# Optimization experiments

Measured on AMD Instinct MI355X. Metric: run time of the kernel, lower is better.

Reference implementation:

```python
import jax, jax.numpy as jnp
import numpy as np

HIDDEN = 1024
HEADS = 16
HEAD_DIM = HIDDEN // HEADS
EPS = 1e-5


def setup_inputs() -> dict:
    key = jax.random.key(0)
    ks = jax.random.split(key, 8)
    B, S, D = 2, 2048, HIDDEN
    s = 1.0 / np.sqrt(D)
    return {
        "x": jax.random.normal(ks[0], (B, S, D), dtype=jnp.float32),
        "Wq": jax.random.uniform(ks[1], (D, D), jnp.float32, -s, s),
        "bq": jnp.zeros((D,), jnp.float32),
        "Wk": jax.random.uniform(ks[2], (D, D), jnp.float32, -s, s),
        "bk": jnp.zeros((D,), jnp.float32),
        "Wv": jax.random.uniform(ks[3], (D, D), jnp.float32, -s, s),
        "bv": jnp.zeros((D,), jnp.float32),
        "gamma": jnp.ones((D,), jnp.float32),
        "beta": jnp.zeros((D,), jnp.float32),
    }


def reference(x, Wq, bq, Wk, bk, Wv, bv, gamma, beta):
    B, S, D = x.shape
    H, Hd = HEADS, HEAD_DIM
    # QKV projections -> [B, H, S, Hd]
    q = (x @ Wq + bq).reshape(B, S, H, Hd).transpose(0, 2, 1, 3)
    k = (x @ Wk + bk).reshape(B, S, H, Hd).transpose(0, 2, 1, 3)
    v = (x @ Wv + bv).reshape(B, S, H, Hd).transpose(0, 2, 1, 3)
    scores = jnp.einsum('bhqd,bhkd->bhqk', q, k) / np.sqrt(Hd).astype(np.float32)
    attn = jax.nn.softmax(scores, axis=-1)  # dropout identity in eval
    ctx = jnp.einsum('bhqk,bhkd->bhqd', attn, v)
    ctx = ctx.transpose(0, 2, 1, 3).reshape(B, S, D)
    y = x + ctx
    mu = jnp.mean(y, axis=-1, keepdims=True)
    var = jnp.var(y, axis=-1, keepdims=True)
    out = (y - mu) * jax.lax.rsqrt(var + EPS) * gamma + beta
    return out, attn.mean(axis=1)
```

## Files before the change

kernel.cpp:

```cpp
#include <hip/hip_runtime.h>

#define S_LEN 2048
#define DIM   1024
#define NH    16
#define HD    64

typedef __bf16 bf16x8 __attribute__((ext_vector_type(8)));
typedef __bf16 bf16x4 __attribute__((ext_vector_type(4)));
typedef float  f32x4  __attribute__((ext_vector_type(4)));
typedef float  f32x16 __attribute__((ext_vector_type(16)));
typedef unsigned int u32x4 __attribute__((ext_vector_type(4)));

#define SCALE_Q (0.125f * 1.44269504088896f)

#define GLOAD_LDS16(g, l) __builtin_amdgcn_global_load_lds( \
    (const __attribute__((address_space(1))) void*)(g),     \
    (__attribute__((address_space(3))) void*)(l), 16, 0, 0)

static __device__ __forceinline__ unsigned cvt_pk_bf16(float a, float b) {
  unsigned r;
  asm("v_cvt_pk_bf16_f32 %0, %1, %2" : "=v"(r) : "v"(a), "v"(b));
  return r;
}

__global__ __launch_bounds__(256) void cast_x_kernel(const float* __restrict__ x,
                                                     __bf16* __restrict__ xb) {
  int i = blockIdx.x * 256 + threadIdx.x;
  const float4 a = ((const float4*)x)[i * 2];
  const float4 b = ((const float4*)x)[i * 2 + 1];
  bf16x8 o;
  o[0] = (__bf16)a.x; o[1] = (__bf16)a.y; o[2] = (__bf16)a.z; o[3] = (__bf16)a.w;
  o[4] = (__bf16)b.x; o[5] = (__bf16)b.y; o[6] = (__bf16)b.z; o[7] = (__bf16)b.w;
  ((bf16x8*)xb)[i] = o;
}

__global__ __launch_bounds__(256) void transW_kernel(const float* __restrict__ Wq,
                                                     const float* __restrict__ Wk,
                                                     const float* __restrict__ Wv,
                                                     __bf16* __restrict__ WT) {
  int which = blockIdx.z;
  const float* W = (which == 0) ? Wq : ((which == 1) ? Wk : Wv);
  __bf16* o = WT + (size_t)which * DIM * DIM;
  __shared__ __bf16 t[64][65];
  int k0 = blockIdx.y * 64, n0 = blockIdx.x * 64;
  int tid = threadIdx.x;
  int c4 = (tid & 15) * 4, rb = tid >> 4;
#pragma unroll
  for (int p = 0; p < 4; ++p) {
    int r = p * 16 + rb;
    float4 a = *(const float4*)&W[(size_t)(k0 + r) * DIM + n0 + c4];
    t[r][c4 + 0] = (__bf16)a.x; t[r][c4 + 1] = (__bf16)a.y;
    t[r][c4 + 2] = (__bf16)a.z; t[r][c4 + 3] = (__bf16)a.w;
  }
  __syncthreads();
#pragma unroll
  for (int p = 0; p < 4; ++p) {
    int n = p * 16 + rb;
    bf16x4 v;
    v[0] = t[c4 + 0][n]; v[1] = t[c4 + 1][n];
    v[2] = t[c4 + 2][n]; v[3] = t[c4 + 3][n];
    *(bf16x4*)&o[(size_t)(n0 + n) * DIM + k0 + c4] = v;
  }
}

__global__ __launch_bounds__(256) void qkv_gemm_kernel(const __bf16* __restrict__ xb,
                                                       const __bf16* __restrict__ WT,
                                                       const float* __restrict__ bq,
                                                       const float* __restrict__ bk,
                                                       const float* __restrict__ bv,
                                                       __bf16* __restrict__ qkv) {
  int which = blockIdx.z;
  const __bf16* Wt = WT + (size_t)which * DIM * DIM;
  const float* bias = (which == 0) ? bq : ((which == 1) ? bk : bv);
  __bf16* outp = qkv + (size_t)which * 2 * NH * S_LEN * HD;
  int m0 = blockIdx.y * 128;
  int n0 = blockIdx.x * 128;
  __shared__ __align__(16) char smem[36864];
  __bf16 (*As)[64] = (__bf16(*)[64])smem;
  __bf16 (*Bs)[64] = (__bf16(*)[64])(smem + 16384);
  __bf16 (*Ct)[136] = (__bf16(*)[136])smem;
  int tid = threadIdx.x;
  int wave = tid >> 6, lane = tid & 63;
  int g = lane >> 4, l15 = lane & 15;
  int wm = (wave >> 1) * 64, wn = (wave & 1) * 64;
  int lr = lane >> 3;
  int lc = (lane & 7) * 8;
  const __bf16* ga = &xb[(size_t)(m0 + wave * 32 + lr) * DIM + lc];
  const __bf16* gb = &Wt[(size_t)(n0 + wave * 32 + lr) * DIM + lc];
  f32x4 acc[4][4] = {};
  for (int k0 = 0; k0 < DIM; k0 += 64) {
#pragma unroll
    for (int c = 0; c < 4; ++c) {
      GLOAD_LDS16(ga + k0 + (size_t)(c * 8) * DIM, &As[wave * 32 + c * 8][0]);
      GLOAD_LDS16(gb + k0 + (size_t)(c * 8) * DIM, &Bs[wave * 32 + c * 8][0]);
    }
    __syncthreads();
#pragma unroll
    for (int ks = 0; ks < 2; ++ks) {
      bf16x8 af[4], bfr[4];
#pragma unroll
      for (int s = 0; s < 4; ++s) {
        af[s]  = *(const bf16x8*)&As[wm + s * 16 + l15][ks * 32 + g * 8];
        bfr[s] = *(const bf16x8*)&Bs[wn + s * 16 + l15][ks * 32 + g * 8];
      }
#pragma unroll
      for (int i = 0; i < 4; ++i)
#pragma unroll
        for (int j = 0; j < 4; ++j)
          acc[i][j] = __builtin_amdgcn_mfma_f32_16x16x32_bf16(af[i], bfr[j], acc[i][j], 0, 0, 0);
    }
    __syncthreads();
  }
  if (which != 2) {
    float scale = (which == 0) ? SCALE_Q : 1.0f;
#pragma unroll
    for (int i = 0; i < 4; ++i)
#pragma unroll
      for (int j = 0; j < 4; ++j) {
        int n = n0 + wn + j * 16 + l15;
        float bval = bias[n];
#pragma unroll
        for (int r = 0; r < 4; ++r) {
          int m = m0 + wm + i * 16 + g * 4 + r;
          float val = (acc[i][j][r] + bval) * scale;
          int bb = m >> 11, ss = m & 2047;
          int hh = n >> 6, hd = n & 63;
          outp[(((size_t)bb * NH + hh) * S_LEN + ss) * HD + hd] = (__bf16)val;
        }
      }
  } else {
#pragma unroll
    for (int i = 0; i < 4; ++i)
#pragma unroll
      for (int j = 0; j < 4; ++j) {
        int nl = wn + j * 16 + l15;
        float bval = bias[n0 + nl];
        bf16x4 t;
#pragma unroll
        for (int r = 0; r < 4; ++r) t[r] = (__bf16)(acc[i][j][r] + bval);
        *(bf16x4*)&Ct[nl][wm + i * 16 + g * 4] = t;
      }
    __syncthreads();
#pragma unroll
    for (int it = 0; it < 8; ++it) {
      int idx = (it * 256 + tid) * 8;
      int row = idx >> 7, col = idx & 127;
      int n = n0 + row, hh = n >> 6, hd = n & 63;
      int m = m0 + col, bb = m >> 11, ss = m & 2047;
      *(bf16x8*)&outp[(((size_t)bb * NH + hh) * HD + hd) * S_LEN + ss] =
          *(const bf16x8*)&Ct[row][col];
    }
  }
}

__global__ __launch_bounds__(512, 4) void attn_flash_kernel(const __bf16* __restrict__ qw,
                                                            const __bf16* __restrict__ kw,
                                                            const __bf16* __restrict__ vtw,
                                                            const float* __restrict__ x,
                                                            float* __restrict__ y,
                                                            float* __restrict__ c_out) {
  int qt = blockIdx.x;
  int h  = blockIdx.y;
  int b  = blockIdx.z;
  size_t hoff = (size_t)(b * NH + h) * S_LEN * HD;
  const __bf16* qh = qw + hoff;
  const __bf16* kh = kw + hoff;
  const __bf16* vth = vtw + hoff;
  __shared__ __align__(16) char smem[66560];
  __bf16 (*Kbase)[64] = (__bf16(*)[64])smem;
  __bf16 (*Vbase)[64] = (__bf16(*)[64])(smem + 32768);
  float (*ctxbuf)[64] = (float(*)[64])smem;
  float* mlbuf = (float*)(smem + 65536);
  int tid = threadIdx.x;
  int wave = tid >> 6, lane = tid & 63;
  int half = wave >> 2, wsub = wave & 3;
  int l31 = lane & 31, hi = lane >> 5;
  int swz = (l31 & 7) << 3;
  int q = qt * 128 + wsub * 32 + l31;
  int qlocal = wsub * 32 + l31;
  bf16x8 qf[4];
#pragma unroll
  for (int ks = 0; ks < 4; ++ks)
    qf[ks] = *(const bf16x8*)&qh[(size_t)q * HD + ks * 16 + hi * 8];
  int st = tid & 255;
  int sr0 = st >> 3;
  int sc  = (st & 7) * 8;
  int swzs = (sr0 & 7) << 3;
  int pl = (sc & 8) ? sc - 4 : sc;
  int ph = (sc & 8) ? sc + 4 : sc + 8;
  bf16x8 kv[2], vv[2];
#pragma unroll
  for (int i = 0; i < 2; ++i) {
    int r = sr0 + i * 32;
    kv[i] = *(const bf16x8*)&kh[(size_t)(half * 64 + r) * HD + sc];
    vv[i] = *(const bf16x8*)&vth[(size_t)r * S_LEN + half * 64 + sc];
  }
  {
    __bf16 (*Kd)[64] = Kbase + half * 64;
    __bf16 (*Vd)[64] = Vbase + half * 64;
#pragma unroll
    for (int i = 0; i < 2; ++i) {
      int r = sr0 + i * 32;
      *(bf16x8*)&Kd[r][sc ^ swzs] = kv[i];
      bf16x4 vlo, vhi4;
#pragma unroll
      for (int e = 0; e < 4; ++e) { vlo[e] = vv[i][e]; vhi4[e] = vv[i][e + 4]; }
      *(bf16x4*)&Vd[r][pl ^ swzs] = vlo;
      *(bf16x4*)&Vd[r][ph ^ swzs] = vhi4;
    }
  }
  {
    int ktn = 2 + half;
#pragma unroll
    for (int i = 0; i < 2; ++i) {
      int r = sr0 + i * 32;
      kv[i] = *(const bf16x8*)&kh[(size_t)(ktn * 64 + r) * HD + sc];
      vv[i] = *(const bf16x8*)&vth[(size_t)r * S_LEN + ktn * 64 + sc];
    }
  }
  float m_r = -1e30f, l_r = 0.f;
  f32x16 ctx0 = {}, ctx1 = {};
  __syncthreads();
  for (int t = 0; t < 16; ++t) {
    int cur = t & 1;
    const __bf16 (*Kc)[64] = (const __bf16(*)[64])(Kbase + cur * 128 + half * 64);
    const __bf16 (*Vc)[64] = (const __bf16(*)[64])(Vbase + cur * 128 + half * 64);
    f32x16 s0 = {}, s1 = {};
    __builtin_amdgcn_s_setprio(1);
#pragma unroll
    for (int ks = 0; ks < 4; ++ks) {
      bf16x8 k0 = *(const bf16x8*)&Kc[l31][(ks * 16 + hi * 8) ^ swz];
      bf16x8 k1 = *(const bf16x8*)&Kc[32 + l31][(ks * 16 + hi * 8) ^ swz];
      s0 = __builtin_amdgcn_mfma_f32_32x32x16_bf16(k0, qf[ks], s0, 0, 0, 0);
      s1 = __builtin_amdgcn_mfma_f32_32x32x16_bf16(k1, qf[ks], s1, 0, 0, 0);
    }
    __builtin_amdgcn_s_setprio(0);
    float vmax = s0[0];
#pragma unroll
    for (int r = 1; r < 16; ++r) vmax = fmaxf(vmax, s0[r]);
#pragma unroll
    for (int r = 0; r < 16; ++r) vmax = fmaxf(vmax, s1[r]);
    vmax = fmaxf(vmax, __shfl_xor(vmax, 32));
    if (__any(vmax > m_r)) {
      float mnew = fmaxf(m_r, vmax);
      float alpha = __builtin_amdgcn_exp2f(m_r - mnew);
      m_r = mnew;
      ctx0 *= alpha; ctx1 *= alpha; l_r *= alpha;
    }
    float ps = 0.f;
#pragma unroll
    for (int r = 0; r < 16; ++r) { s0[r] = __builtin_amdgcn_exp2f(s0[r] - m_r); ps += s0[r]; }
#pragma unroll
    for (int r = 0; r < 16; ++r) { s1[r] = __builtin_amdgcn_exp2f(s1[r] - m_r); ps += s1[r]; }
    ps += __shfl_xor(ps, 32);
    l_r += ps;
    bf16x8 pa[4];
#pragma unroll
    for (int f = 0; f < 2; ++f) {
      u32x4 tt;
#pragma unroll
      for (int j = 0; j < 4; ++j) tt[j] = cvt_pk_bf16(s0[f * 8 + 2 * j], s0[f * 8 + 2 * j + 1]);
      pa[f] = __builtin_bit_cast(bf16x8, tt);
    }
#pragma unroll
    for (int f = 0; f < 2; ++f) {
      u32x4 tt;
#pragma unroll
      for (int j = 0; j < 4; ++j) tt[j] = cvt_pk_bf16(s1[f * 8 + 2 * j], s1[f * 8 + 2 * j + 1]);
      pa[2 + f] = __builtin_bit_cast(bf16x8, tt);
    }
    __builtin_amdgcn_s_setprio(1);
#pragma unroll
    for (int f = 0; f < 4; ++f) {
      bf16x8 v0 = *(const bf16x8*)&Vc[l31][(f * 16 + hi * 8) ^ swz];
      bf16x8 v1 = *(const bf16x8*)&Vc[32 + l31][(f * 16 + hi * 8) ^ swz];
      ctx0 = __builtin_amdgcn_mfma_f32_32x32x16_bf16(v0, pa[f], ctx0, 0, 0, 0);
      ctx1 = __builtin_amdgcn_mfma_f32_32x32x16_bf16(v1, pa[f], ctx1, 0, 0, 0);
    }
    __builtin_amdgcn_s_setprio(0);
    if (t < 15) {
      __bf16 (*Kd)[64] = Kbase + (cur ^ 1) * 128 + half * 64;
      __bf16 (*Vd)[64] = Vbase + (cur ^ 1) * 128 + half * 64;
#pragma unroll
      for (int i = 0; i < 2; ++i) {
        int r = sr0 + i * 32;
        *(bf16x8*)&Kd[r][sc ^ swzs] = kv[i];
        bf16x4 vlo, vhi4;
#pragma unroll
        for (int e = 0; e < 4; ++e) { vlo[e] = vv[i][e]; vhi4[e] = vv[i][e + 4]; }
        *(bf16x4*)&Vd[r][pl ^ swzs] = vlo;
        *(bf16x4*)&Vd[r][ph ^ swzs] = vhi4;
      }
      if (t < 14) {
        int ktn = 2 * (t + 2) + half;
#pragma unroll
        for (int i = 0; i < 2; ++i) {
          int r = sr0 + i * 32;
          kv[i] = *(const bf16x8*)&kh[(size_t)(ktn * 64 + r) * HD + sc];
          vv[i] = *(const bf16x8*)&vth[(size_t)r * S_LEN + ktn * 64 + sc];
        }
      }
    }
    __syncthreads();
  }
  int sw2 = (qlocal & 7) << 2;
  if (half == 1) {
#pragma unroll
    for (int rq = 0; rq < 4; ++rq) {
      int hd0 = rq * 8 + hi * 4;
      f32x4 a, bb;
#pragma unroll
      for (int j = 0; j < 4; ++j) { a[j] = ctx0[rq * 4 + j]; bb[j] = ctx1[rq * 4 + j]; }
      *(f32x4*)&ctxbuf[qlocal][hd0 ^ sw2] = a;
      *(f32x4*)&ctxbuf[qlocal][(32 + hd0) ^ sw2] = bb;
    }
    if (hi == 0) { mlbuf[qlocal] = m_r; mlbuf[128 + qlocal] = l_r; }
  }
  __syncthreads();
  if (half == 0) {
    float m1 = mlbuf[qlocal], l1 = mlbuf[128 + qlocal];
    float m = fmaxf(m_r, m1);
    float a0 = __builtin_amdgcn_exp2f(m_r - m);
    float a1 = __builtin_amdgcn_exp2f(m1 - m);
    float l = a0 * l_r + a1 * l1;
    float il = 1.0f / l;
    float cvl = m + __builtin_amdgcn_logf(l);
    if (lane < 32)
      c_out[(size_t)(b * NH + h) * S_LEN + qt * 128 + wsub * 32 + lane] = cvl;
    size_t ybase = ((size_t)b * S_LEN + q) * DIM + h * HD;
#pragma unroll
    for (int rq = 0; rq < 4; ++rq) {
      int hd0 = rq * 8 + hi * 4;
      f32x4 c1 = *(const f32x4*)&ctxbuf[qlocal][hd0 ^ sw2];
      float4 xv0 = *(const float4*)&x[ybase + hd0];
      float4 o0;
      o0.x = xv0.x + (a0 * ctx0[rq * 4 + 0] + a1 * c1[0]) * il;
      o0.y = xv0.y + (a0 * ctx0[rq * 4 + 1] + a1 * c1[1]) * il;
      o0.z = xv0.z + (a0 * ctx0[rq * 4 + 2] + a1 * c1[2]) * il;
      o0.w = xv0.w + (a0 * ctx0[rq * 4 + 3] + a1 * c1[3]) * il;
      *(float4*)&y[ybase + hd0] = o0;
      int hd1 = 32 + hd0;
      f32x4 c2 = *(const f32x4*)&ctxbuf[qlocal][hd1 ^ sw2];
      float4 xv1 = *(const float4*)&x[ybase + hd1];
      float4 o1;
      o1.x = xv1.x + (a0 * ctx1[rq * 4 + 0] + a1 * c2[0]) * il;
      o1.y = xv1.y + (a0 * ctx1[rq * 4 + 1] + a1 * c2[1]) * il;
      o1.z = xv1.z + (a0 * ctx1[rq * 4 + 2] + a1 * c2[2]) * il;
      o1.w = xv1.w + (a0 * ctx1[rq * 4 + 3] + a1 * c2[3]) * il;
      *(float4*)&y[ybase + hd1] = o1;
    }
  }
}

__global__ __launch_bounds__(256) void attn_mean_kernel(const __bf16* __restrict__ qw,
                                                        const __bf16* __restrict__ kw,
                                                        const float* __restrict__ c_in,
                                                        float* __restrict__ out_mean) {
  int kt = blockIdx.x, qt = blockIdx.y, b = blockIdx.z;
  __shared__ __align__(16) __bf16 Ks[2][64][64];
  int tid = threadIdx.x;
  int wave = tid >> 6, lane = tid & 63;
  int l31 = lane & 31, hi = lane >> 5;
  int swz = (l31 & 7) << 3;
  int q = qt * 128 + wave * 32 + l31;
  const __bf16* qp = qw + (size_t)b * NH * S_LEN * HD;
  const __bf16* kp = kw + (size_t)b * NH * S_LEN * HD;
  const float*  cp = c_in + (size_t)b * NH * S_LEN + q;
  int sr0 = tid >> 3;
  int sc  = (tid & 7) * 8;
  int swzs = (sr0 & 7) << 3;
  bf16x8 kv[2];
#pragma unroll
  for (int i = 0; i < 2; ++i)
    kv[i] = *(const bf16x8*)&kp[(size_t)(kt * 64 + sr0 + i * 32) * HD + sc];
#pragma unroll
  for (int i = 0; i < 2; ++i)
    *(bf16x8*)&Ks[0][sr0 + i * 32][sc ^ swzs] = kv[i];
#pragma unroll
  for (int i = 0; i < 2; ++i)
    kv[i] = *(const bf16x8*)&kp[S_LEN * HD + (size_t)(kt * 64 + sr0 + i * 32) * HD + sc];
  bf16x8 qc[4], qn[4];
#pragma unroll
  for (int ks = 0; ks < 4; ++ks) {
    qc[ks] = *(const bf16x8*)&qp[(size_t)q * HD + ks * 16 + hi * 8];
    qn[ks] = *(const bf16x8*)&qp[(size_t)S_LEN * HD + (size_t)q * HD + ks * 16 + hi * 8];
  }
  float c_c = cp[0], c_n = cp[S_LEN];
  f32x16 macc0 = {}, macc1 = {};
  __syncthreads();
  for (int h = 0; h < NH; ++h) {
    int cur = h & 1;
    f32x16 s0 = {}, s1 = {};
    __builtin_amdgcn_s_setprio(1);
#pragma unroll
    for (int ks = 0; ks < 4; ++ks) {
      bf16x8 k0 = *(const bf16x8*)&Ks[cur][l31][(ks * 16 + hi * 8) ^ swz];
      bf16x8 k1 = *(const bf16x8*)&Ks[cur][32 + l31][(ks * 16 + hi * 8) ^ swz];
      s0 = __builtin_amdgcn_mfma_f32_32x32x16_bf16(k0, qc[ks], s0, 0, 0, 0);
      s1 = __builtin_amdgcn_mfma_f32_32x32x16_bf16(k1, qc[ks], s1, 0, 0, 0);
    }
    __builtin_amdgcn_s_setprio(0);
    if (h < NH - 1) {
#pragma unroll
      for (int i = 0; i < 2; ++i)
        *(bf16x8*)&Ks[cur ^ 1][sr0 + i * 32][sc ^ swzs] = kv[i];
      if (h < NH - 2) {
        size_t hbn = (size_t)(h + 2) * S_LEN * HD;
#pragma unroll
        for (int i = 0; i < 2; ++i)
          kv[i] = *(const bf16x8*)&kp[hbn + (size_t)(kt * 64 + sr0 + i * 32) * HD + sc];
      }
    }
#pragma unroll
    for (int r = 0; r < 16; ++r) macc0[r] += __builtin_amdgcn_exp2f(s0[r] - c_c);
#pragma unroll
    for (int r = 0; r < 16; ++r) macc1[r] += __builtin_amdgcn_exp2f(s1[r] - c_c);
#pragma unroll
    for (int ks = 0; ks < 4; ++ks) qc[ks] = qn[ks];
    c_c = c_n;
    if (h < NH - 2) {
      size_t hbn = (size_t)(h + 2) * S_LEN * HD;
#pragma unroll
      for (int ks = 0; ks < 4; ++ks)
        qn[ks] = *(const bf16x8*)&qp[hbn + (size_t)q * HD + ks * 16 + hi * 8];
      c_n = cp[(size_t)(h + 2) * S_LEN];
    }
    __syncthreads();
  }
  const float invh = 1.0f / (float)NH;
  size_t obase = ((size_t)b * S_LEN + q) * S_LEN + kt * 64;
#pragma unroll
  for (int rq = 0; rq < 4; ++rq) {
    int k0i = rq * 8 + hi * 4;
    float4 o0;
    o0.x = macc0[rq * 4 + 0] * invh; o0.y = macc0[rq * 4 + 1] * invh;
    o0.z = macc0[rq * 4 + 2] * invh; o0.w = macc0[rq * 4 + 3] * invh;
    *(float4*)&out_mean[obase + k0i] = o0;
    float4 o1;
    o1.x = macc1[rq * 4 + 0] * invh; o1.y = macc1[rq * 4 + 1] * invh;
    o1.z = macc1[rq * 4 + 2] * invh; o1.w = macc1[rq * 4 + 3] * invh;
    *(float4*)&out_mean[obase + 32 + k0i] = o1;
  }
}

__global__ __launch_bounds__(256) void ln_kernel(const float* __restrict__ y,
                                                 const float* __restrict__ gamma,
                                                 const float* __restrict__ beta,
                                                 float* __restrict__ out) {
  int row = blockIdx.x;
  const float* yr = y + (size_t)row * DIM;
  int tid = threadIdx.x;
  float4 v = *(const float4*)&yr[tid * 4];
  float s = v.x + v.y + v.z + v.w;
  float sq = v.x * v.x + v.y * v.y + v.z * v.z + v.w * v.w;
#pragma unroll
  for (int off = 1; off < 64; off <<= 1) {
    s += __shfl_xor(s, off);
    sq += __shfl_xor(sq, off);
  }
  __shared__ float red[8];
  int wave = tid >> 6, lane = tid & 63;
  if (lane == 0) { red[wave] = s; red[4 + wave] = sq; }
  __syncthreads();
  s = red[0] + red[1] + red[2] + red[3];
  sq = red[4] + red[5] + red[6] + red[7];
  float mu = s * (1.0f / DIM);
  float var = sq * (1.0f / DIM) - mu * mu;
  float rstd = rsqrtf(var + 1e-5f);
  float* orow = out + (size_t)row * DIM;
  float4 gv = *(const float4*)&gamma[tid * 4];
  float4 bv = *(const float4*)&beta[tid * 4];
  float4 ov;
  ov.x = (v.x - mu) * rstd * gv.x + bv.x;
  ov.y = (v.y - mu) * rstd * gv.y + bv.y;
  ov.z = (v.z - mu) * rstd * gv.z + bv.z;
  ov.w = (v.w - mu) * rstd * gv.w + bv.w;
  *(float4*)&orow[tid * 4] = ov;
}

extern "C" void kernel_launch(void* const* d_in, const int* in_sizes, int n_in,
                              void* d_out, int out_size, void* d_ws, size_t ws_size,
                              hipStream_t stream) {
  const float* x  = (const float*)d_in[0];
  const float* Wq = (const float*)d_in[1];
  const float* bq = (const float*)d_in[2];
  const float* Wk = (const float*)d_in[3];
  const float* bk = (const float*)d_in[4];
  const float* Wv = (const float*)d_in[5];
  const float* bv = (const float*)d_in[6];
  const float* gamma = (const float*)d_in[7];
  const float* beta  = (const float*)d_in[8];
  float* out = (float*)d_out;

  char* ws = (char*)d_ws;
  __bf16* xb   = (__bf16*)ws;
  __bf16* WT   = (__bf16*)(ws + 8388608);
  __bf16* qkv  = (__bf16*)(ws + 14680064);
  float*  y    = (float*)(ws + 39845888);
  float*  c_ws = (float*)(ws + 56623104);

  cast_x_kernel<<<2048, 256, 0, stream>>>(x, xb);
  transW_kernel<<<dim3(16, 16, 3), 256, 0, stream>>>(Wq, Wk, Wv, WT);
  qkv_gemm_kernel<<<dim3(8, 32, 3), 256, 0, stream>>>(xb, WT, bq, bk, bv, qkv);
  attn_flash_kernel<<<dim3(16, 16, 2), 512, 0, stream>>>(qkv, qkv + 4194304, qkv + 8388608,
                                                         x, y, c_ws);
  attn_mean_kernel<<<dim3(32, 16, 2), 256, 0, stream>>>(qkv, qkv + 4194304, c_ws,
                                                        out + 4194304);
  ln_kernel<<<4096, 256, 0, stream>>>(y, gamma, beta, out);
}
```

Baseline: 182.3 us.

## Software-pipeline attention loop so next QK^T overlaps current PV and softmax

Restructures the flash-attention main loop so the QK^T MFMA for tile t+1 is issued before the PV MFMA for tile t, and softmax for the next tile runs after the current PV. K is prefetched one tile further ahead than V, with separate global-load and LDS-store stages per operand. The loop is fully unrolled and the softmax logic is moved into a macro. The aim is to hide softmax VALU and exp latency behind matrix-core work, at the cost of more live registers (extra score accumulators) and a larger unrolled code body that could reduce occupancy.

```diff
diff --git a/kernel.cpp b/kernel.cpp
--- a/kernel.cpp
+++ b/kernel.cpp
@@ -153,6 +153,39 @@
   }
 }
 
+#define SOFTMAX_PACK(S0, S1, PA)                                                        \
+  {                                                                                     \
+    float vmax = S0[0];                                                                 \
+    _Pragma("unroll") for (int r = 1; r < 16; ++r) vmax = fmaxf(vmax, S0[r]);           \
+    _Pragma("unroll") for (int r = 0; r < 16; ++r) vmax = fmaxf(vmax, S1[r]);           \
+    vmax = fmaxf(vmax, __shfl_xor(vmax, 32));                                           \
+    if (__any(vmax > m_r)) {                                                            \
+      float mnew = fmaxf(m_r, vmax);                                                    \
+      float alpha = __builtin_amdgcn_exp2f(m_r - mnew);                                 \
+      m_r = mnew;                                                                       \
+      ctx0 *= alpha; ctx1 *= alpha; l_r *= alpha;                                       \
+    }                                                                                   \
+    float ps = 0.f;                                                                     \
+    _Pragma("unroll") for (int r = 0; r < 16; ++r) {                                    \
+      S0[r] = __builtin_amdgcn_exp2f(S0[r] - m_r); ps += S0[r]; }                       \
+    _Pragma("unroll") for (int r = 0; r < 16; ++r) {                                    \
+      S1[r] = __builtin_amdgcn_exp2f(S1[r] - m_r); ps += S1[r]; }                       \
+    ps += __shfl_xor(ps, 32);                                                           \
+    l_r += ps;                                                                          \
+    _Pragma("unroll") for (int f = 0; f < 2; ++f) {                                     \
+      u32x4 tt;                                                                         \
+      _Pragma("unroll") for (int j = 0; j < 4; ++j)                                     \
+        tt[j] = cvt_pk_bf16(S0[f * 8 + 2 * j], S0[f * 8 + 2 * j + 1]);                  \
+      PA[f] = __builtin_bit_cast(bf16x8, tt);                                           \
+    }                                                                                   \
+    _Pragma("unroll") for (int f = 0; f < 2; ++f) {                                     \
+      u32x4 tt;                                                                         \
+      _Pragma("unroll") for (int j = 0; j < 4; ++j)                                     \
+        tt[j] = cvt_pk_bf16(S1[f * 8 + 2 * j], S1[f * 8 + 2 * j + 1]);                  \
+      PA[2 + f] = __builtin_bit_cast(bf16x8, tt);                                       \
+    }                                                                                   \
+  }
+
 __global__ __launch_bounds__(512, 4) void attn_flash_kernel(const __bf16* __restrict__ qw,
                                                             const __bf16* __restrict__ kw,
                                                             const __bf16* __restrict__ vtw,
@@ -189,43 +222,50 @@
   int pl = (sc & 8) ? sc - 4 : sc;
   int ph = (sc & 8) ? sc + 4 : sc + 8;
   bf16x8 kv[2], vv[2];
-#pragma unroll
-  for (int i = 0; i < 2; ++i) {
-    int r = sr0 + i * 32;
-    kv[i] = *(const bf16x8*)&kh[(size_t)(half * 64 + r) * HD + sc];
-    vv[i] = *(const bf16x8*)&vth[(size_t)r * S_LEN + half * 64 + sc];
-  }
+
+#pragma unroll
+  for (int i = 0; i < 2; ++i)
+    kv[i] = *(const bf16x8*)&kh[(size_t)(half * 64 + sr0 + i * 32) * HD + sc];
   {
     __bf16 (*Kd)[64] = Kbase + half * 64;
+#pragma unroll
+    for (int i = 0; i < 2; ++i) *(bf16x8*)&Kd[sr0 + i * 32][sc ^ swzs] = kv[i];
+  }
+#pragma unroll
+  for (int i = 0; i < 2; ++i)
+    kv[i] = *(const bf16x8*)&kh[(size_t)((2 + half) * 64 + sr0 + i * 32) * HD + sc];
+  {
+    __bf16 (*Kd)[64] = Kbase + 128 + half * 64;
+#pragma unroll
+    for (int i = 0; i < 2; ++i) *(bf16x8*)&Kd[sr0 + i * 32][sc ^ swzs] = kv[i];
+  }
+#pragma unroll
+  for (int i = 0; i < 2; ++i)
+    vv[i] = *(const bf16x8*)&vth[(size_t)(sr0 + i * 32) * S_LEN + half * 64 + sc];
+  {
     __bf16 (*Vd)[64] = Vbase + half * 64;
 #pragma unroll
     for (int i = 0; i < 2; ++i) {
-      int r = sr0 + i * 32;
-      *(bf16x8*)&Kd[r][sc ^ swzs] = kv[i];
       bf16x4 vlo, vhi4;
 #pragma unroll
       for (int e = 0; e < 4; ++e) { vlo[e] = vv[i][e]; vhi4[e] = vv[i][e + 4]; }
-      *(bf16x4*)&Vd[r][pl ^ swzs] = vlo;
-      *(bf16x4*)&Vd[r][ph ^ swzs] = vhi4;
-    }
-  }
-  {
-    int ktn = 2 + half;
-#pragma unroll
-    for (int i = 0; i < 2; ++i) {
-      int r = sr0 + i * 32;
-      kv[i] = *(const bf16x8*)&kh[(size_t)(ktn * 64 + r) * HD + sc];
-      vv[i] = *(const bf16x8*)&vth[(size_t)r * S_LEN + ktn * 64 + sc];
-    }
-  }
+      *(bf16x4*)&Vd[sr0 + i * 32][pl ^ swzs] = vlo;
+      *(bf16x4*)&Vd[sr0 + i * 32][ph ^ swzs] = vhi4;
+    }
+  }
+#pragma unroll
+  for (int i = 0; i < 2; ++i) {
+    kv[i] = *(const bf16x8*)&kh[(size_t)((4 + half) * 64 + sr0 + i * 32) * HD + sc];
+    vv[i] = *(const bf16x8*)&vth[(size_t)(sr0 + i * 32) * S_LEN + (2 + half) * 64 + sc];
+  }
+  __syncthreads();
+
   float m_r = -1e30f, l_r = 0.f;
   f32x16 ctx0 = {}, ctx1 = {};
-  __syncthreads();
-  for (int t = 0; t < 16; ++t) {
-    int cur = t & 1;
-    const __bf16 (*Kc)[64] = (const __bf16(*)[64])(Kbase + cur * 128 + half * 64);
-    const __bf16 (*Vc)[64] = (const __bf16(*)[64])(Vbase + cur * 128 + half * 64);
+  bf16x8 pa[4];
+  {
     f32x16 s0 = {}, s1 = {};
+    const __bf16 (*Kc)[64] = (const __bf16(*)[64])(Kbase + half * 64);
     __builtin_amdgcn_s_setprio(1);
 #pragma unroll
     for (int ks = 0; ks < 4; ++ks) {
@@ -235,71 +275,65 @@
       s1 = __builtin_amdgcn_mfma_f32_32x32x16_bf16(k1, qf[ks], s1, 0, 0, 0);
     }
     __builtin_amdgcn_s_setprio(0);
-    float vmax = s0[0];
-#pragma unroll
-    for (int r = 1; r < 16; ++r) vmax = fmaxf(vmax, s0[r]);
-#pragma unroll
-    for (int r = 0; r < 16; ++r) vmax = fmaxf(vmax, s1[r]);
-    vmax = fmaxf(vmax, __shfl_xor(vmax, 32));
-    if (__any(vmax > m_r)) {
-      float mnew = fmaxf(m_r, vmax);
-      float alpha = __builtin_amdgcn_exp2f(m_r - mnew);
-      m_r = mnew;
-      ctx0 *= alpha; ctx1 *= alpha; l_r *= alpha;
-    }
-    float ps = 0.f;
-#pragma unroll
-    for (int r = 0; r < 16; ++r) { s0[r] = __builtin_amdgcn_exp2f(s0[r] - m_r); ps += s0[r]; }
-#pragma unroll
-    for (int r = 0; r < 16; ++r) { s1[r] = __builtin_amdgcn_exp2f(s1[r] - m_r); ps += s1[r]; }
-    ps += __shfl_xor(ps, 32);
-    l_r += ps;
-    bf16x8 pa[4];
-#pragma unroll
-    for (int f = 0; f < 2; ++f) {
-      u32x4 tt;
-#pragma unroll
-      for (int j = 0; j < 4; ++j) tt[j] = cvt_pk_bf16(s0[f * 8 + 2 * j], s0[f * 8 + 2 * j + 1]);
-      pa[f] = __builtin_bit_cast(bf16x8, tt);
-    }
-#pragma unroll
-    for (int f = 0; f < 2; ++f) {
-      u32x4 tt;
-#pragma unroll
-      for (int j = 0; j < 4; ++j) tt[j] = cvt_pk_bf16(s1[f * 8 + 2 * j], s1[f * 8 + 2 * j + 1]);
-      pa[2 + f] = __builtin_bit_cast(bf16x8, tt);
-    }
-    __builtin_amdgcn_s_setprio(1);
-#pragma unroll
-    for (int f = 0; f < 4; ++f) {
-      bf16x8 v0 = *(const bf16x8*)&Vc[l31][(f * 16 + hi * 8) ^ swz];
-      bf16x8 v1 = *(const bf16x8*)&Vc[32 + l31][(f * 16 + hi * 8) ^ swz];
-      ctx0 = __builtin_amdgcn_mfma_f32_32x32x16_bf16(v0, pa[f], ctx0, 0, 0, 0);
-      ctx1 = __builtin_amdgcn_mfma_f32_32x32x16_bf16(v1, pa[f], ctx1, 0, 0, 0);
-    }
-    __builtin_amdgcn_s_setprio(0);
+    SOFTMAX_PACK(s0, s1, pa);
+  }
+  __syncthreads();
+
+#pragma unroll
+  for (int t = 0; t < 16; ++t) {
+    f32x16 sn0 = {}, sn1 = {};
     if (t < 15) {
-      __bf16 (*Kd)[64] = Kbase + (cur ^ 1) * 128 + half * 64;
-      __bf16 (*Vd)[64] = Vbase + (cur ^ 1) * 128 + half * 64;
+      const __bf16 (*Kc)[64] = (const __bf16(*)[64])(Kbase + ((t + 1) & 1) * 128 + half * 64);
+      __builtin_amdgcn_s_setprio(1);
+#pragma unroll
+      for (int ks = 0; ks < 4; ++ks) {
+        bf16x8 k0 = *(const bf16x8*)&Kc[l31][(ks * 16 + hi * 8) ^ swz];
+        bf16x8 k1 = *(const bf16x8*)&Kc[32 + l31][(ks * 16 + hi * 8) ^ swz];
+        sn0 = __builtin_amdgcn_mfma_f32_32x32x16_bf16(k0, qf[ks], sn0, 0, 0, 0);
+        sn1 = __builtin_amdgcn_mfma_f32_32x32x16_bf16(k1, qf[ks], sn1, 0, 0, 0);
+      }
+      __builtin_amdgcn_s_setprio(0);
+    }
+    {
+      const __bf16 (*Vc)[64] = (const __bf16(*)[64])(Vbase + (t & 1) * 128 + half * 64);
+      __builtin_amdgcn_s_setprio(1);
+#pragma unroll
+      for (int f = 0; f < 4; ++f) {
+        bf16x8 v0 = *(const bf16x8*)&Vc[l31][(f * 16 + hi * 8) ^ swz];
+        bf16x8 v1 = *(const bf16x8*)&Vc[32 + l31][(f * 16 + hi * 8) ^ swz];
+        ctx0 = __builtin_amdgcn_mfma_f32_32x32x16_bf16(v0, pa[f], ctx0, 0, 0, 0);
+        ctx1 = __builtin_amdgcn_mfma_f32_32x32x16_bf16(v1, pa[f], ctx1, 0, 0, 0);
+      }
+      __builtin_amdgcn_s_setprio(0);
+    }
+    if (t < 14) {
+      __bf16 (*Kd)[64] = Kbase + (t & 1) * 128 + half * 64;
+#pragma unroll
+      for (int i = 0; i < 2; ++i) *(bf16x8*)&Kd[sr0 + i * 32][sc ^ swzs] = kv[i];
+    }
+    if (t < 15) {
+      __bf16 (*Vd)[64] = Vbase + ((t + 1) & 1) * 128 + half * 64;
 #pragma unroll
       for (int i = 0; i < 2; ++i) {
-        int r = sr0 + i * 32;
-        *(bf16x8*)&Kd[r][sc ^ swzs] = kv[i];
         bf16x4 vlo, vhi4;
 #pragma unroll
         for (int e = 0; e < 4; ++e) { vlo[e] = vv[i][e]; vhi4[e] = vv[i][e + 4]; }
-        *(bf16x4*)&Vd[r][pl ^ swzs] = vlo;
-        *(bf16x4*)&Vd[r][ph ^ swzs] = vhi4;
-      }
-      if (t < 14) {
-        int ktn = 2 * (t + 2) + half;
-#pragma unroll
-        for (int i = 0; i < 2; ++i) {
-          int r = sr0 + i * 32;
-          kv[i] = *(const bf16x8*)&kh[(size_t)(ktn * 64 + r) * HD + sc];
-          vv[i] = *(const bf16x8*)&vth[(size_t)r * S_LEN + ktn * 64 + sc];
-        }
-      }
+        *(bf16x4*)&Vd[sr0 + i * 32][pl ^ swzs] = vlo;
+        *(bf16x4*)&Vd[sr0 + i * 32][ph ^ swzs] = vhi4;
+      }
+    }
+    if (t < 13) {
+#pragma unroll
+      for (int i = 0; i < 2; ++i)
+        kv[i] = *(const bf16x8*)&kh[(size_t)((2 * (t + 3) + half) * 64 + sr0 + i * 32) * HD + sc];
+    }
+    if (t < 14) {
+#pragma unroll
+      for (int i = 0; i < 2; ++i)
+        vv[i] = *(const bf16x8*)&vth[(size_t)(sr0 + i * 32) * S_LEN + (2 * (t + 2) + half) * 64 + sc];
+    }
+    if (t < 15) {
+      SOFTMAX_PACK(sn0, sn1, pa);
     }
     __syncthreads();
   }
```

Measured after the change: 191.8 us. 1.05x slower.
